# Kernel tuning notes

Measured on AMD Instinct MI355X. Metric: run time of the kernel, lower is better.

## Reference

```python
import jax, jax.numpy as jnp
import numpy as np
from jax import lax

NPOINT = 1024
RADIUS = 0.4
NSAMPLE = 32
BN_EPS = 1e-5


def _square_distance(src, dst):
    # src [B,S,3], dst [B,N,3] -> [B,S,N]
    d = -2.0 * jnp.einsum('bsc,bnc->bsn', src, dst)
    d = d + jnp.sum(src ** 2, -1)[:, :, None]
    d = d + jnp.sum(dst ** 2, -1)[:, None, :]
    return d


def _farthest_point_sample(xyz, npoint):
    # xyz [B,N,3] -> int32 indices [B,npoint]
    B, N, _ = xyz.shape
    # deterministic start at index 0 (torch uses randint; math is otherwise identical)
    init_far = jnp.zeros((B,), dtype=jnp.int32)
    init_dist = jnp.full((B, N), 1e10, dtype=xyz.dtype)

    def step(carry, _):
        distance, farthest = carry
        centroid = jnp.take_along_axis(xyz, farthest[:, None, None], axis=1)  # [B,1,3]
        dist = jnp.sum((xyz - centroid) ** 2, -1)  # [B,N]
        distance = jnp.minimum(distance, dist)
        new_far = jnp.argmax(distance, axis=-1).astype(jnp.int32)
        return (distance, new_far), farthest

    (_, _), cents = lax.scan(step, (init_dist, init_far), None, length=npoint)
    return cents.T  # [B, npoint]


def _query_ball_point(radius, nsample, xyz, new_xyz):
    # xyz [B,N,3], new_xyz [B,S,3] -> idx [B,S,nsample]
    B, N, _ = xyz.shape
    sqr = _square_distance(new_xyz, xyz)  # [B,S,N]
    ar = jnp.arange(N, dtype=jnp.int32)
    gi = jnp.where(sqr > radius * radius, N, ar[None, None, :])
    gi = jnp.sort(gi, axis=-1)[:, :, :nsample]
    first = gi[:, :, :1]
    return jnp.where(gi == N, first, gi)


def setup_inputs() -> dict:
    key = jax.random.key(0)
    ks = jax.random.split(key, 8)
    B, N = 16, 4096
    inp = {
        'xyz': jax.random.normal(ks[0], (B, 3, N), jnp.float32),
        'points': jax.random.normal(ks[1], (B, 6, N), jnp.float32),
    }
    dims = [(64, 9), (64, 64), (128, 64)]
    for i, (o, c) in enumerate(dims):
        inp[f'w{i}'] = jax.random.normal(ks[2 + i], (o, c), jnp.float32) * 0.05
        inp[f'b{i}'] = jnp.zeros((o,), jnp.float32)
        inp[f'g{i}'] = jnp.ones((o,), jnp.float32)
        inp[f'beta{i}'] = jnp.zeros((o,), jnp.float32)
    return inp


def reference(xyz, points, w0, b0, g0, beta0, w1, b1, g1, beta1, w2, b2, g2, beta2):
    # xyz [B,3,N], points [B,6,N]
    xyz_t = jnp.transpose(xyz, (0, 2, 1))      # [B,N,3]
    pts_t = jnp.transpose(points, (0, 2, 1))   # [B,N,6]
    B, N, _ = xyz_t.shape
    S, ns = NPOINT, NSAMPLE

    fps_idx = _farthest_point_sample(xyz_t, S)                 # [B,S]
    new_xyz = jnp.take_along_axis(xyz_t, fps_idx[:, :, None], axis=1)  # [B,S,3]
    idx = _query_ball_point(RADIUS, ns, xyz_t, new_xyz)        # [B,S,ns]
    flat = idx.reshape(B, S * ns, 1)
    g_xyz = jnp.take_along_axis(xyz_t, flat, axis=1).reshape(B, S, ns, 3)
    g_xyz = g_xyz - new_xyz[:, :, None, :]                     # grouped_xyz_norm
    g_pts = jnp.take_along_axis(pts_t, flat, axis=1).reshape(B, S, ns, -1)
    feat = jnp.concatenate([g_xyz, g_pts], axis=-1)            # [B,S,ns,9]

    # shared MLP: 1x1 conv + BatchNorm (training-mode batch stats) + ReLU
    for w, b, g, be in ((w0, b0, g0, beta0), (w1, b1, g1, beta1), (w2, b2, g2, beta2)):
        h = jnp.einsum('bsnc,oc->bsno', feat, w) + b
        mu = jnp.mean(h, axis=(0, 1, 2))
        var = jnp.var(h, axis=(0, 1, 2))
        feat = jax.nn.relu((h - mu) * lax.rsqrt(var + BN_EPS) * g + be)

    new_points = jnp.max(feat, axis=2)                         # max over nsample -> [B,S,Cout]
    return (jnp.transpose(new_xyz, (0, 2, 1)), jnp.transpose(new_points, (0, 2, 1)))
```

## Files before the change

kernel.cpp:

```cpp
#include <hip/hip_runtime.h>
#include <hip/hip_bf16.h>
#include <stdint.h>

#define NB 16
#define NP 4096
#define NSP 1024
#define KNN 32
#define PTOT (NB*NSP*KNN)
#define NTILES (PTOT/16)

typedef __attribute__((ext_vector_type(8))) short short8;
typedef __attribute__((ext_vector_type(4))) float f32x4;
typedef __attribute__((ext_vector_type(2))) float f32x2;

__device__ __forceinline__ float fadd_(float a,float b){return __fadd_rn(a,b);}
__device__ __forceinline__ float fmul_(float a,float b){return __fmul_rn(a,b);}
__device__ __forceinline__ float fsub_(float a,float b){return __fsub_rn(a,b);}

__device__ __forceinline__ float bf2f(unsigned short u){
    unsigned int x = ((unsigned int)u) << 16; float f; __builtin_memcpy(&f,&x,4); return f;
}
__device__ __forceinline__ unsigned short f2bf(float f){
    unsigned int x; __builtin_memcpy(&x,&f,4);
    x = x + 0x7fffu + ((x>>16)&1u);
    return (unsigned short)(x>>16);
}

template<int CTRL>
__device__ __forceinline__ float dpp_fmax_step(float v){
    int d = __builtin_amdgcn_update_dpp(0, __float_as_int(v), CTRL, 0xF, 0xF, true);
    return fmaxf(v, __int_as_float(d));
}

__device__ __forceinline__ void ab_from_stats(const double* __restrict__ st, const float* __restrict__ g,
    const float* __restrict__ beta, int o, float* A_out, float* B_out)
{
    double s=0.0, q=0.0;
#pragma unroll
    for (int slot=0;slot<8;slot++){
        s += st[(size_t)(slot*2+0)*128+o];
        q += st[(size_t)(slot*2+1)*128+o];
    }
    const double cnt = (double)PTOT;
    float mean = (float)(s/cnt);
    float var  = (float)(q/cnt - (s/cnt)*(s/cnt));
    float inv  = rsqrtf(var + 1e-5f);
    float A = g[o]*inv;
    *A_out = A; *B_out = beta[o] - mean*A;
}

__global__ __launch_bounds__(256,1) void fps_kernel(const float* __restrict__ xyz,
    float* __restrict__ new_xyz, float* __restrict__ out0)
{
    const int b = blockIdx.x, tid = threadIdx.x;
    const int lane = tid & 63, wv = tid >> 6;
    const float* xb = xyz + (size_t)b*3*NP;
    __shared__ float4 sp[NP];
    __shared__ unsigned long long slots[2][4];
    __shared__ int lds_far[NSP];
    f32x2 px[8], py[8], pz[8], pd2[8];
    const int base = tid*16;
#pragma unroll
    for (int j=0;j<16;j+=4){
        float4 vx = *(const float4*)(xb + base + j);
        float4 vy = *(const float4*)(xb + NP + base + j);
        float4 vz = *(const float4*)(xb + 2*NP + base + j);
        px[j/2]   = (f32x2){vx.x,vx.y}; px[j/2+1] = (f32x2){vx.z,vx.w};
        py[j/2]   = (f32x2){vy.x,vy.y}; py[j/2+1] = (f32x2){vy.z,vy.w};
        pz[j/2]   = (f32x2){vz.x,vz.y}; pz[j/2+1] = (f32x2){vz.z,vz.w};
        sp[base+j+0] = make_float4(vx.x,vy.x,vz.x,0.f);
        sp[base+j+1] = make_float4(vx.y,vy.y,vz.y,0.f);
        sp[base+j+2] = make_float4(vx.z,vy.z,vz.z,0.f);
        sp[base+j+3] = make_float4(vx.w,vy.w,vz.w,0.f);
        pd2[j/2]   = (f32x2){1e10f,1e10f};
        pd2[j/2+1] = (f32x2){1e10f,1e10f};
    }
    __syncthreads();
    int far = 0;
    float cx, cy, cz;
    { float4 c0 = sp[0]; cx=c0.x; cy=c0.y; cz=c0.z; }
    for (int s=0;s<NSP;s++){
        if (tid == (s & 255)) lds_far[s] = far;
        f32x2 bm2 = (f32x2){-1.f,-1.f};
        {
#pragma clang fp contract(off)
            const f32x2 cx2 = (f32x2){cx,cx}, cy2 = (f32x2){cy,cy}, cz2 = (f32x2){cz,cz};
#pragma unroll
            for (int k=0;k<8;k++){
                f32x2 dx = px[k]-cx2, dy = py[k]-cy2, dz = pz[k]-cz2;
                f32x2 d  = (dx*dx + dy*dy) + dz*dz;
                pd2[k] = __builtin_elementwise_min(pd2[k], d);
                bm2    = __builtin_elementwise_max(bm2, pd2[k]);
            }
        }
        float bd = fmaxf(bm2.x, bm2.y);
        float m = bd;
        m = dpp_fmax_step<0x111>(m);
        m = dpp_fmax_step<0x112>(m);
        m = dpp_fmax_step<0x114>(m);
        m = dpp_fmax_step<0x118>(m);
        m = dpp_fmax_step<0x142>(m);
        m = dpp_fmax_step<0x143>(m);
        const float wm = __int_as_float(__builtin_amdgcn_readlane(__float_as_int(m), 63));
        int il = 0;
#pragma unroll
        for (int k=7;k>=0;k--){
            if (pd2[k].y == wm) il = 2*k+1;
            if (pd2[k].x == wm) il = 2*k;
        }
        unsigned long long wmask = __ballot(bd == wm);
        int L = __ffsll(wmask) - 1;
        int widx = __builtin_amdgcn_readlane(base + il, L);
        unsigned long long key = ((unsigned long long)__float_as_uint(wm) << 32)
                               | (unsigned int)(NP-1-widx);
        if (lane==0) slots[s&1][wv] = key;
        __syncthreads();
        {
            const unsigned long long* sl = slots[s&1];
            unsigned long long a0 = sl[0], a1 = sl[1], a2 = sl[2], a3 = sl[3];
            unsigned long long m0 = a0>a1?a0:a1, m1 = a2>a3?a2:a3;
            unsigned long long mx = m0>m1?m0:m1;
            far = NP-1-(int)(mx & 0xFFFFFFFFu);
        }
        float4 c = sp[far]; cx=c.x; cy=c.y; cz=c.z;
    }
    __syncthreads();
    for (int i=tid;i<NSP;i+=256){
        int id = lds_far[i];
        float4 c = sp[id];
        float* nz = new_xyz + ((size_t)b*NSP + i)*3;
        nz[0]=c.x; nz[1]=c.y; nz[2]=c.z;
        out0[(size_t)b*3*NSP + i]         = c.x;
        out0[(size_t)b*3*NSP + NSP + i]   = c.y;
        out0[(size_t)b*3*NSP + 2*NSP + i] = c.z;
    }
}

__global__ __launch_bounds__(256,1) void ball_gather_kernel(const float* __restrict__ xyz,
    const float* __restrict__ pts, const float* __restrict__ new_xyz,
    unsigned short* __restrict__ feat)
{
    const int lane = threadIdx.x & 63, wv = threadIdx.x >> 6;
    const int center = blockIdx.x*4 + wv;
    const int b = center >> 10;
    const float* xb = xyz + (size_t)b*3*NP;
    const float* pb = pts + (size_t)b*6*NP;
    const float* nz = new_xyz + (size_t)center*3;
    const float cx=nz[0], cy=nz[1], cz=nz[2];
    const float src2 = fadd_(fadd_(fmul_(cx,cx),fmul_(cy,cy)),fmul_(cz,cz));
    const float R2 = (float)(0.4*0.4);
    __shared__ int slots[4][32];
    int total = 0;
    for (int c0=0;c0<NP;c0+=64){
        const int i = c0 + lane;
        float x=xb[i], y=xb[NP+i], z=xb[2*NP+i];
        float dot  = fadd_(fadd_(fmul_(cx,x),fmul_(cy,y)),fmul_(cz,z));
        float dst2 = fadd_(fadd_(fmul_(x,x),fmul_(y,y)),fmul_(z,z));
        float d = fadd_(fadd_(fmul_(-2.0f,dot), src2), dst2);
        bool pred = !(d > R2);
        unsigned long long m = __ballot(pred);
        int pos = total + (int)__popcll(m & ((1ull<<lane)-1ull));
        if (pred && pos < 32) slots[wv][pos] = i;
        total += (int)__popcll(m);
        if (total >= 32) break;
    }
    const int nvalid = total < 32 ? total : 32;
    const int n = lane & 31;
    const int idx = slots[wv][ (n < nvalid) ? n : 0 ];
    unsigned short* fr = feat + (size_t)center*KNN*32 + (size_t)n*32;
    if (lane < 32){
        float gx = fsub_(xb[idx], cx), gy = fsub_(xb[NP+idx], cy), gz = fsub_(xb[2*NP+idx], cz);
        float p0=pb[idx], p1=pb[NP+idx], p2=pb[2*NP+idx], p3=pb[3*NP+idx], p4=pb[4*NP+idx];
        short8 v;
        v[0]=(short)f2bf(gx); v[1]=(short)f2bf(gy); v[2]=(short)f2bf(gz);
        v[3]=(short)f2bf(p0); v[4]=(short)f2bf(p1); v[5]=(short)f2bf(p2);
        v[6]=(short)f2bf(p3); v[7]=(short)f2bf(p4);
        *(short8*)fr = v;
    } else {
        float p5 = pb[5*NP+idx];
        short8 v = (short8){0,0,0,0,0,0,0,0};
        v[0]=(short)f2bf(p5);
        *(short8*)(fr+8)  = v;
        short8 z8 = (short8){0,0,0,0,0,0,0,0};
        *(short8*)(fr+16) = z8;
        *(short8*)(fr+24) = z8;
    }
}

template<int KT,int OT,bool NORM_IN,bool STORE_H>
__global__ __launch_bounds__(256,1) void conv_kernel(const unsigned short* __restrict__ in,
    const unsigned short* __restrict__ wp, const float* __restrict__ bias,
    const double* __restrict__ stats_in, const float* __restrict__ gin,
    const float* __restrict__ bein,
    unsigned short* __restrict__ h_out, double* __restrict__ stats)
{
    constexpr int K = KT*32, O = OT*16;
    const int lane = threadIdx.x & 63, wv = threadIdx.x >> 6;
    const int col = lane & 15, quad = lane >> 4;
    __shared__ float sA[128], sB[128];
    if constexpr (NORM_IN){
        if ((int)threadIdx.x < K){
            float A, B;
            ab_from_stats(stats_in, gin, bein, threadIdx.x, &A, &B);
            sA[threadIdx.x] = A; sB[threadIdx.x] = B;
        }
        __syncthreads();
    }
    short8 bf[OT][KT];
#pragma unroll
    for (int t=0;t<OT;t++)
#pragma unroll
        for (int kt=0;kt<KT;kt++)
            bf[t][kt] = *(const short8*)(wp + (size_t)(t*16+col)*K + kt*32 + quad*8);
    float brow[OT];
#pragma unroll
    for (int t=0;t<OT;t++) brow[t] = bias[t*16+col];
    float nA[KT*8], nB[KT*8];
    if constexpr (NORM_IN){
#pragma unroll
        for (int kt=0;kt<KT;kt++)
#pragma unroll
            for (int j=0;j<8;j++){
                int c = kt*32+quad*8+j;
                nA[kt*8+j]=sA[c]; nB[kt*8+j]=sB[c];
            }
    }
    float ssum[OT], ssq[OT];
#pragma unroll
    for (int t=0;t<OT;t++){ ssum[t]=0.f; ssq[t]=0.f; }
    const int gw = blockIdx.x*4 + wv, nw = gridDim.x*4;
    for (int tile=gw; tile<NTILES; tile+=nw){
        const int row0 = tile*16;
        short8 af[KT];
#pragma unroll
        for (int kt=0;kt<KT;kt++){
            af[kt] = *(const short8*)(in + (size_t)(row0+col)*K + kt*32 + quad*8);
            if constexpr (NORM_IN){
#pragma unroll
                for (int j=0;j<8;j++){
                    float x = bf2f((unsigned short)af[kt][j]);
                    x = fmaxf(x*nA[kt*8+j]+nB[kt*8+j], 0.f);
                    af[kt][j] = (short)f2bf(x);
                }
            }
        }
        f32x4 acc[OT];
#pragma unroll
        for (int t=0;t<OT;t++) acc[t] = (f32x4){0.f,0.f,0.f,0.f};
#pragma unroll
        for (int kt=0;kt<KT;kt++)
#pragma unroll
            for (int t=0;t<OT;t++)
                acc[t] = __builtin_amdgcn_mfma_f32_16x16x32_bf16(af[kt], bf[t][kt], acc[t], 0,0,0);
#pragma unroll
        for (int t=0;t<OT;t++){
#pragma unroll
            for (int r=0;r<4;r++){
                float h = acc[t][r] + brow[t];
                if constexpr (STORE_H)
                    h_out[(size_t)(row0 + quad*4 + r)*O + t*16 + col] = f2bf(h);
                ssum[t] += h; ssq[t] = fmaf(h,h,ssq[t]);
            }
        }
    }
    __shared__ float bsum[128], bssq[128];
    for (int i=threadIdx.x;i<128;i+=256){ bsum[i]=0.f; bssq[i]=0.f; }
    __syncthreads();
#pragma unroll
    for (int t=0;t<OT;t++){
        float v = ssum[t]; v += __shfl_xor(v,16,64); v += __shfl_xor(v,32,64);
        float q = ssq[t];  q += __shfl_xor(q,16,64); q += __shfl_xor(q,32,64);
        if (quad==0){ atomicAdd(&bsum[t*16+col], v); atomicAdd(&bssq[t*16+col], q); }
    }
    __syncthreads();
    if ((int)threadIdx.x < O){
        const int slot = blockIdx.x & 7;
        atomicAdd(&stats[(size_t)(slot*2+0)*128 + threadIdx.x], (double)bsum[threadIdx.x]);
        atomicAdd(&stats[(size_t)(slot*2+1)*128 + threadIdx.x], (double)bssq[threadIdx.x]);
    }
}

__global__ __launch_bounds__(256,1) void conv01_kernel(
    const unsigned short* __restrict__ feat,
    const unsigned short* __restrict__ wp0, const float* __restrict__ b0v,
    const double* __restrict__ stats0, const float* __restrict__ g0v,
    const float* __restrict__ be0v,
    const unsigned short* __restrict__ wp1, const float* __restrict__ b1v,
    unsigned short* __restrict__ h1_out, double* __restrict__ stats1)
{
    const int lane = threadIdx.x & 63, wv = threadIdx.x >> 6;
    const int col = lane & 15, quad = lane >> 4;
    __shared__ float sA[64], sB[64];
    __shared__ unsigned short scratch[4][16*72];
    if ((int)threadIdx.x < 64){
        float A, B;
        ab_from_stats(stats0, g0v, be0v, threadIdx.x, &A, &B);
        sA[threadIdx.x] = A; sB[threadIdx.x] = B;
    }
    __syncthreads();
    short8 bf0[4];
#pragma unroll
    for (int t=0;t<4;t++)
        bf0[t] = *(const short8*)(wp0 + (size_t)(t*16+col)*32 + quad*8);
    short8 bf1[4][2];
#pragma unroll
    for (int t=0;t<4;t++)
#pragma unroll
        for (int kt=0;kt<2;kt++)
            bf1[t][kt] = *(const short8*)(wp1 + (size_t)(t*16+col)*64 + kt*32 + quad*8);
    float b0row[4], n0A[4], n0B[4], b1row[4];
#pragma unroll
    for (int t=0;t<4;t++){
        b0row[t] = b0v[t*16+col];
        n0A[t]   = sA[t*16+col];
        n0B[t]   = sB[t*16+col];
        b1row[t] = b1v[t*16+col];
    }
    float ssum[4], ssq[4];
#pragma unroll
    for (int t=0;t<4;t++){ ssum[t]=0.f; ssq[t]=0.f; }
    unsigned short* sw = scratch[wv];
    const int gw = blockIdx.x*4 + wv, nw = gridDim.x*4;
    for (int tile=gw; tile<NTILES; tile+=nw){
        const int row0 = tile*16;
        short8 af0 = *(const short8*)(feat + (size_t)(row0+col)*32 + quad*8);
        f32x4 acc0[4];
#pragma unroll
        for (int t=0;t<4;t++) acc0[t] = (f32x4){0.f,0.f,0.f,0.f};
#pragma unroll
        for (int t=0;t<4;t++)
            acc0[t] = __builtin_amdgcn_mfma_f32_16x16x32_bf16(af0, bf0[t], acc0[t], 0,0,0);
#pragma unroll
        for (int t=0;t<4;t++)
#pragma unroll
            for (int r=0;r<4;r++){
                float h = acc0[t][r] + b0row[t];
                unsigned short hb = f2bf(h);
                float x = fmaxf(bf2f(hb)*n0A[t] + n0B[t], 0.f);
                sw[(quad*4+r)*72 + t*16 + col] = f2bf(x);
            }
        short8 af1[2];
        af1[0] = *(const short8*)(&sw[(size_t)col*72 + quad*8]);
        af1[1] = *(const short8*)(&sw[(size_t)col*72 + 32 + quad*8]);
        f32x4 acc1[4];
#pragma unroll
        for (int t=0;t<4;t++) acc1[t] = (f32x4){0.f,0.f,0.f,0.f};
#pragma unroll
        for (int kt=0;kt<2;kt++)
#pragma unroll
            for (int t=0;t<4;t++)
                acc1[t] = __builtin_amdgcn_mfma_f32_16x16x32_bf16(af1[kt], bf1[t][kt], acc1[t], 0,0,0);
#pragma unroll
        for (int t=0;t<4;t++)
#pragma unroll
            for (int r=0;r<4;r++){
                float h = acc1[t][r] + b1row[t];
                h1_out[(size_t)(row0 + quad*4 + r)*64 + t*16 + col] = f2bf(h);
                ssum[t] += h; ssq[t] = fmaf(h,h,ssq[t]);
            }
    }
    __shared__ float bsum[64], bssq[64];
    for (int i=threadIdx.x;i<64;i+=256){ bsum[i]=0.f; bssq[i]=0.f; }
    __syncthreads();
#pragma unroll
    for (int t=0;t<4;t++){
        float v = ssum[t]; v += __shfl_xor(v,16,64); v += __shfl_xor(v,32,64);
        float q = ssq[t];  q += __shfl_xor(q,16,64); q += __shfl_xor(q,32,64);
        if (quad==0){ atomicAdd(&bsum[t*16+col], v); atomicAdd(&bssq[t*16+col], q); }
    }
    __syncthreads();
    if ((int)threadIdx.x < 64){
        const int slot = blockIdx.x & 7;
        atomicAdd(&stats1[(size_t)(slot*2+0)*128 + threadIdx.x], (double)bsum[threadIdx.x]);
        atomicAdd(&stats1[(size_t)(slot*2+1)*128 + threadIdx.x], (double)bssq[threadIdx.x]);
    }
}

__global__ __launch_bounds__(256,1) void conv_final_kernel(const unsigned short* __restrict__ in,
    const unsigned short* __restrict__ wp, const float* __restrict__ bias,
    const double* __restrict__ stats1, const float* __restrict__ g1v,
    const float* __restrict__ be1v,
    const double* __restrict__ stats2, const float* __restrict__ g2v,
    const float* __restrict__ be2v,
    float* __restrict__ out1)
{
    constexpr int KT=2, OT=8, K=64;
    const int lane = threadIdx.x & 63, wv = threadIdx.x >> 6;
    const int col = lane & 15, quad = lane >> 4;
    __shared__ float sInA[64], sInB[64], sOutA[128], sOutB[128];
    {
        const int t0 = threadIdx.x;
        if (t0 < 128){
            float A, B;
            ab_from_stats(stats2, g2v, be2v, t0, &A, &B);
            sOutA[t0] = A; sOutB[t0] = B;
        } else if (t0 < 192){
            float A, B;
            ab_from_stats(stats1, g1v, be1v, t0-128, &A, &B);
            sInA[t0-128] = A; sInB[t0-128] = B;
        }
        __syncthreads();
    }
    short8 bf[OT][KT];
#pragma unroll
    for (int t=0;t<OT;t++)
#pragma unroll
        for (int kt=0;kt<KT;kt++)
            bf[t][kt] = *(const short8*)(wp + (size_t)(t*16+col)*K + kt*32 + quad*8);
    float brow[OT], oA[OT], oB[OT];
#pragma unroll
    for (int t=0;t<OT;t++){
        brow[t] = bias[t*16+col];
        oA[t] = sOutA[t*16+col];
        oB[t] = sOutB[t*16+col];
    }
    float nA[16], nB[16];
#pragma unroll
    for (int kt=0;kt<2;kt++)
#pragma unroll
        for (int j=0;j<8;j++){
            int c = kt*32+quad*8+j;
            nA[kt*8+j]=sInA[c]; nB[kt*8+j]=sInB[c];
        }
    const int gw = blockIdx.x*4 + wv, nw = gridDim.x*4;
    for (int grp=gw; grp<NB*NSP; grp+=nw){
        float vmax[OT];
#pragma unroll
        for (int t=0;t<OT;t++) vmax[t]=0.f;
#pragma unroll
        for (int mt=0; mt<2; mt++){
            const int row0 = grp*32 + mt*16;
            short8 af[KT];
#pragma unroll
            for (int kt=0;kt<2;kt++){
                af[kt] = *(const short8*)(in + (size_t)(row0+col)*K + kt*32 + quad*8);
#pragma unroll
                for (int j=0;j<8;j++){
                    float x = bf2f((unsigned short)af[kt][j]);
                    x = fmaxf(x*nA[kt*8+j]+nB[kt*8+j], 0.f);
                    af[kt][j] = (short)f2bf(x);
                }
            }
            f32x4 acc[OT];
#pragma unroll
            for (int t=0;t<OT;t++) acc[t] = (f32x4){0.f,0.f,0.f,0.f};
#pragma unroll
            for (int kt=0;kt<2;kt++)
#pragma unroll
                for (int t=0;t<OT;t++)
                    acc[t] = __builtin_amdgcn_mfma_f32_16x16x32_bf16(af[kt], bf[t][kt], acc[t], 0,0,0);
#pragma unroll
            for (int t=0;t<OT;t++){
#pragma unroll
                for (int r=0;r<4;r++){
                    float h = acc[t][r] + brow[t];
                    float x = fmaxf(h*oA[t]+oB[t], 0.f);
                    vmax[t] = fmaxf(vmax[t], x);
                }
            }
        }
#pragma unroll
        for (int t=0;t<OT;t++){
            float v = vmax[t];
            v = fmaxf(v, __shfl_xor(v,16,64));
            v = fmaxf(v, __shfl_xor(v,32,64));
            if (quad==0){
                int o = t*16+col, bb = grp>>10, ss = grp&1023;
                out1[((size_t)bb*128+o)*NSP + ss] = v;
            }
        }
    }
}

__global__ void prep_kernel(const float* __restrict__ w0, const float* __restrict__ w1,
    const float* __restrict__ w2, unsigned short* __restrict__ wp0,
    unsigned short* __restrict__ wp1, unsigned short* __restrict__ wp2)
{
    int t = blockIdx.x*256 + threadIdx.x;
    if (t < 64*32){ int o=t>>5, c=t&31; wp0[t] = (c<9) ? f2bf(w0[o*9+c]) : (unsigned short)0; }
    if (t < 64*64)  wp1[t] = f2bf(w1[t]);
    if (t < 128*64) wp2[t] = f2bf(w2[t]);
}

extern "C" void kernel_launch(void* const* d_in, const int* in_sizes, int n_in,
                              void* d_out, int out_size, void* d_ws, size_t ws_size,
                              hipStream_t stream)
{
    (void)in_sizes; (void)n_in; (void)out_size; (void)ws_size;
    const float* xyz = (const float*)d_in[0];
    const float* pts = (const float*)d_in[1];
    const float* w0  = (const float*)d_in[2];
    const float* b0  = (const float*)d_in[3];
    const float* g0  = (const float*)d_in[4];
    const float* be0 = (const float*)d_in[5];
    const float* w1  = (const float*)d_in[6];
    const float* b1  = (const float*)d_in[7];
    const float* g1  = (const float*)d_in[8];
    const float* be1 = (const float*)d_in[9];
    const float* w2  = (const float*)d_in[10];
    const float* b2  = (const float*)d_in[11];
    const float* g2  = (const float*)d_in[12];
    const float* be2 = (const float*)d_in[13];

    char* ws = (char*)d_ws;
    size_t off = 0;
    auto alloc = [&](size_t sz)->char*{ char* p = ws + off; off = (off + sz + 255) & ~(size_t)255; return p; };
    float*          new_xyz = (float*)         alloc((size_t)NB*NSP*3*4);
    unsigned short* wp0     = (unsigned short*)alloc(64*32*2);
    unsigned short* wp1     = (unsigned short*)alloc(64*64*2);
    unsigned short* wp2     = (unsigned short*)alloc(128*64*2);
    double*         stats   = (double*)        alloc((size_t)3*8*2*128*8);
    unsigned short* feat    = (unsigned short*)alloc((size_t)PTOT*32*2);
    unsigned short* h1      = (unsigned short*)alloc((size_t)PTOT*64*2);

    float* out0 = (float*)d_out;
    float* out1 = out0 + (size_t)NB*3*NSP;

    hipMemsetAsync(stats, 0, (size_t)3*8*2*128*8, stream);
    prep_kernel<<<32,256,0,stream>>>(w0,w1,w2,wp0,wp1,wp2);
    fps_kernel<<<NB,256,0,stream>>>(xyz, new_xyz, out0);
    ball_gather_kernel<<<NB*NSP/4,256,0,stream>>>(xyz, pts, new_xyz, feat);
    conv_kernel<1,4,false,false><<<1024,256,0,stream>>>(feat, wp0, b0, nullptr, nullptr, nullptr, nullptr, stats);
    conv01_kernel<<<1024,256,0,stream>>>(feat, wp0, b0, stats, g0, be0, wp1, b1, h1, stats + 2048);
    conv_kernel<2,8,true,false><<<1024,256,0,stream>>>(h1, wp2, b2, stats + 2048, g1, be1, nullptr, stats + 4096);
    conv_final_kernel<<<2048,256,0,stream>>>(h1, wp2, b2, stats + 2048, g1, be1, stats + 4096, g2, be2, out1);
}
```

Before: 860.8 us.

## Fuse layer-3 conv stats pass with pooling via per-group max/min of pre-BN output

Layer 3 no longer runs a separate stats-only conv pass followed by a second conv pass. A single pass computes the layer-3 conv, accumulates the BN sums, and records the per-group max and min of the pre-normalisation outputs. A small finalize kernel then applies the affine BN and ReLU, choosing max or min by the sign of the scale, since the affine map is monotonic. This removes one full read of h1 and one set of MFMA work, but writes two extra 8 MB buffers and adds a kernel launch.

```diff
diff --git a/kernel.cpp b/kernel.cpp
--- a/kernel.cpp
+++ b/kernel.cpp
@@ -8,6 +8,7 @@
 #define KNN 32
 #define PTOT (NB*NSP*KNN)
 #define NTILES (PTOT/16)
+#define NGRP (NB*NSP)
 
 typedef __attribute__((ext_vector_type(8))) short short8;
 typedef __attribute__((ext_vector_type(4))) float f32x4;
@@ -376,44 +377,34 @@
     }
 }
 
-__global__ __launch_bounds__(256,1) void conv_final_kernel(const unsigned short* __restrict__ in,
-    const unsigned short* __restrict__ wp, const float* __restrict__ bias,
+__global__ __launch_bounds__(256,1) void conv2_stats_pool_kernel(
+    const unsigned short* __restrict__ in,
+    const unsigned short* __restrict__ wp,
+    const float* __restrict__ bias,
     const double* __restrict__ stats1, const float* __restrict__ g1v,
     const float* __restrict__ be1v,
-    const double* __restrict__ stats2, const float* __restrict__ g2v,
-    const float* __restrict__ be2v,
-    float* __restrict__ out1)
+    double* __restrict__ stats2,
+    float* __restrict__ hmax, float* __restrict__ hmin)
 {
     constexpr int KT=2, OT=8, K=64;
     const int lane = threadIdx.x & 63, wv = threadIdx.x >> 6;
     const int col = lane & 15, quad = lane >> 4;
-    __shared__ float sInA[64], sInB[64], sOutA[128], sOutB[128];
-    {
-        const int t0 = threadIdx.x;
-        if (t0 < 128){
-            float A, B;
-            ab_from_stats(stats2, g2v, be2v, t0, &A, &B);
-            sOutA[t0] = A; sOutB[t0] = B;
-        } else if (t0 < 192){
-            float A, B;
-            ab_from_stats(stats1, g1v, be1v, t0-128, &A, &B);
-            sInA[t0-128] = A; sInB[t0-128] = B;
-        }
-        __syncthreads();
-    }
+    __shared__ float sInA[64], sInB[64];
+    if ((int)threadIdx.x < 64){
+        float A, B;
+        ab_from_stats(stats1, g1v, be1v, threadIdx.x, &A, &B);
+        sInA[threadIdx.x] = A; sInB[threadIdx.x] = B;
+    }
+    __syncthreads();
     short8 bf[OT][KT];
 #pragma unroll
     for (int t=0;t<OT;t++)
 #pragma unroll
         for (int kt=0;kt<KT;kt++)
             bf[t][kt] = *(const short8*)(wp + (size_t)(t*16+col)*K + kt*32 + quad*8);
-    float brow[OT], oA[OT], oB[OT];
-#pragma unroll
-    for (int t=0;t<OT;t++){
-        brow[t] = bias[t*16+col];
-        oA[t] = sOutA[t*16+col];
-        oB[t] = sOutB[t*16+col];
-    }
+    float brow[OT];
+#pragma unroll
+    for (int t=0;t<OT;t++) brow[t] = bias[t*16+col];
     float nA[16], nB[16];
 #pragma unroll
     for (int kt=0;kt<2;kt++)
@@ -422,11 +413,14 @@
             int c = kt*32+quad*8+j;
             nA[kt*8+j]=sInA[c]; nB[kt*8+j]=sInB[c];
         }
+    float ssum[OT], ssq[OT];
+#pragma unroll
+    for (int t=0;t<OT;t++){ ssum[t]=0.f; ssq[t]=0.f; }
     const int gw = blockIdx.x*4 + wv, nw = gridDim.x*4;
-    for (int grp=gw; grp<NB*NSP; grp+=nw){
-        float vmax[OT];
-#pragma unroll
-        for (int t=0;t<OT;t++) vmax[t]=0.f;
+    for (int grp=gw; grp<NGRP; grp+=nw){
+        float hmx[OT], hmn[OT];
+#pragma unroll
+        for (int t=0;t<OT;t++){ hmx[t]=-3.402823466e38f; hmn[t]=3.402823466e38f; }
 #pragma unroll
         for (int mt=0; mt<2; mt++){
             const int row0 = grp*32 + mt*16;
@@ -454,21 +448,64 @@
 #pragma unroll
                 for (int r=0;r<4;r++){
                     float h = acc[t][r] + brow[t];
-                    float x = fmaxf(h*oA[t]+oB[t], 0.f);
-                    vmax[t] = fmaxf(vmax[t], x);
+                    ssum[t] += h; ssq[t] = fmaf(h,h,ssq[t]);
+                    hmx[t] = fmaxf(hmx[t], h);
+                    hmn[t] = fminf(hmn[t], h);
                 }
             }
         }
 #pragma unroll
         for (int t=0;t<OT;t++){
-            float v = vmax[t];
-            v = fmaxf(v, __shfl_xor(v,16,64));
-            v = fmaxf(v, __shfl_xor(v,32,64));
+            float x = hmx[t];
+            x = fmaxf(x, __shfl_xor(x,16,64));
+            x = fmaxf(x, __shfl_xor(x,32,64));
+            float n = hmn[t];
+            n = fminf(n, __shfl_xor(n,16,64));
+            n = fminf(n, __shfl_xor(n,32,64));
             if (quad==0){
-                int o = t*16+col, bb = grp>>10, ss = grp&1023;
-                out1[((size_t)bb*128+o)*NSP + ss] = v;
-            }
-        }
+                hmax[(size_t)grp*128 + t*16+col] = x;
+                hmin[(size_t)grp*128 + t*16+col] = n;
+            }
+        }
+    }
+    __shared__ float bsum[128], bssq[128];
+    for (int i=threadIdx.x;i<128;i+=256){ bsum[i]=0.f; bssq[i]=0.f; }
+    __syncthreads();
+#pragma unroll
+    for (int t=0;t<OT;t++){
+        float v = ssum[t]; v += __shfl_xor(v,16,64); v += __shfl_xor(v,32,64);
+        float q = ssq[t];  q += __shfl_xor(q,16,64); q += __shfl_xor(q,32,64);
+        if (quad==0){ atomicAdd(&bsum[t*16+col], v); atomicAdd(&bssq[t*16+col], q); }
+    }
+    __syncthreads();
+    if ((int)threadIdx.x < 128){
+        const int slot = blockIdx.x & 7;
+        atomicAdd(&stats2[(size_t)(slot*2+0)*128 + threadIdx.x], (double)bsum[threadIdx.x]);
+        atomicAdd(&stats2[(size_t)(slot*2+1)*128 + threadIdx.x], (double)bssq[threadIdx.x]);
+    }
+}
+
+__global__ __launch_bounds__(256,1) void pool_finalize_kernel(
+    const double* __restrict__ stats2, const float* __restrict__ g2v,
+    const float* __restrict__ be2v,
+    const float* __restrict__ hmax, const float* __restrict__ hmin,
+    float* __restrict__ out1)
+{
+    const int blk = blockIdx.x;
+    const int bb = blk >> 7, o = blk & 127;
+    __shared__ float sAB[2];
+    if (threadIdx.x == 0){
+        float A, B;
+        ab_from_stats(stats2, g2v, be2v, o, &A, &B);
+        sAB[0] = A; sAB[1] = B;
+    }
+    __syncthreads();
+    const float A = sAB[0], B = sAB[1];
+    for (int ss = threadIdx.x; ss < NSP; ss += 256){
+        const size_t g = (size_t)bb*NSP + ss;
+        float mx = hmax[g*128 + o], mn = hmin[g*128 + o];
+        float sel = (A >= 0.f) ? mx : mn;
+        out1[((size_t)bb*128 + o)*NSP + ss] = fmaxf(fmaf(sel, A, B), 0.f);
     }
 }
 
@@ -510,6 +547,8 @@
     unsigned short* wp1     = (unsigned short*)alloc(64*64*2);
     unsigned short* wp2     = (unsigned short*)alloc(128*64*2);
     double*         stats   = (double*)        alloc((size_t)3*8*2*128*8);
+    float*          hmax    = (float*)         alloc((size_t)NGRP*128*4);
+    float*          hmin    = (float*)         alloc((size_t)NGRP*128*4);
     unsigned short* feat    = (unsigned short*)alloc((size_t)PTOT*32*2);
     unsigned short* h1      = (unsigned short*)alloc((size_t)PTOT*64*2);
 
@@ -522,6 +561,6 @@
     ball_gather_kernel<<<NB*NSP/4,256,0,stream>>>(xyz, pts, new_xyz, feat);
     conv_kernel<1,4,false,false><<<1024,256,0,stream>>>(feat, wp0, b0, nullptr, nullptr, nullptr, nullptr, stats);
     conv01_kernel<<<1024,256,0,stream>>>(feat, wp0, b0, stats, g0, be0, wp1, b1, h1, stats + 2048);
-    conv_kernel<2,8,true,false><<<1024,256,0,stream>>>(h1, wp2, b2, stats + 2048, g1, be1, nullptr, stats + 4096);
-    conv_final_kernel<<<2048,256,0,stream>>>(h1, wp2, b2, stats + 2048, g1, be1, stats + 4096, g2, be2, out1);
-}
+    conv2_stats_pool_kernel<<<1024,256,0,stream>>>(h1, wp2, b2, stats + 2048, g1, be1, stats + 4096, hmax, hmin);
+    pool_finalize_kernel<<<NB*128,256,0,stream>>>(stats + 4096, g2, be2, hmax, hmin, out1);
+}
```

Result: no change. 871.6 us (+1.3%).

## Fuse layer-0 BatchNorm statistics into ball-gather kernel via MFMA

Applied to the files above, without the earlier changes.

The ball query and gather kernel now also runs the first 1x1 conv on the gathered features, using MFMA on an LDS copy of each center's 32x32 tile. It reduces per-channel sum and sum-of-squares through shuffles, LDS atomics and global double atomics. This removes the separate stats-only conv pass over feat, saving a full launch and a re-read of feat. In exchange the gather kernel does more work, uses more LDS, and issues more global atomics.

```diff
diff --git a/kernel.cpp b/kernel.cpp
--- a/kernel.cpp
+++ b/kernel.cpp
@@ -138,7 +138,8 @@
 
 __global__ __launch_bounds__(256,1) void ball_gather_kernel(const float* __restrict__ xyz,
     const float* __restrict__ pts, const float* __restrict__ new_xyz,
-    unsigned short* __restrict__ feat)
+    const unsigned short* __restrict__ wp0, const float* __restrict__ b0v,
+    unsigned short* __restrict__ feat, double* __restrict__ stats0)
 {
     const int lane = threadIdx.x & 63, wv = threadIdx.x >> 6;
     const int center = blockIdx.x*4 + wv;
@@ -149,7 +150,16 @@
     const float cx=nz[0], cy=nz[1], cz=nz[2];
     const float src2 = fadd_(fadd_(fmul_(cx,cx),fmul_(cy,cy)),fmul_(cz,cz));
     const float R2 = (float)(0.4*0.4);
+    const int col = lane & 15, quad = lane >> 4;
     __shared__ int slots[4][32];
+    __shared__ unsigned short ftile[4][32*40];
+    short8 bf0[4];
+#pragma unroll
+    for (int t=0;t<4;t++)
+        bf0[t] = *(const short8*)(wp0 + (size_t)(t*16+col)*32 + quad*8);
+    float brow[4];
+#pragma unroll
+    for (int t=0;t<4;t++) brow[t] = b0v[t*16+col];
     int total = 0;
     for (int c0=0;c0<NP;c0+=64){
         const int i = c0 + lane;
@@ -168,6 +178,7 @@
     const int n = lane & 31;
     const int idx = slots[wv][ (n < nvalid) ? n : 0 ];
     unsigned short* fr = feat + (size_t)center*KNN*32 + (size_t)n*32;
+    unsigned short* ft = ftile[wv];
     if (lane < 32){
         float gx = fsub_(xb[idx], cx), gy = fsub_(xb[NP+idx], cy), gz = fsub_(xb[2*NP+idx], cz);
         float p0=pb[idx], p1=pb[NP+idx], p2=pb[2*NP+idx], p3=pb[3*NP+idx], p4=pb[4*NP+idx];
@@ -176,14 +187,53 @@
         v[3]=(short)f2bf(p0); v[4]=(short)f2bf(p1); v[5]=(short)f2bf(p2);
         v[6]=(short)f2bf(p3); v[7]=(short)f2bf(p4);
         *(short8*)fr = v;
+        *(short8*)(&ft[n*40]) = v;
     } else {
         float p5 = pb[5*NP+idx];
         short8 v = (short8){0,0,0,0,0,0,0,0};
         v[0]=(short)f2bf(p5);
+        short8 z8 = (short8){0,0,0,0,0,0,0,0};
         *(short8*)(fr+8)  = v;
-        short8 z8 = (short8){0,0,0,0,0,0,0,0};
         *(short8*)(fr+16) = z8;
         *(short8*)(fr+24) = z8;
+        *(short8*)(&ft[n*40+8])  = v;
+        *(short8*)(&ft[n*40+16]) = z8;
+        *(short8*)(&ft[n*40+24]) = z8;
+    }
+    float ssum[4], ssq[4];
+#pragma unroll
+    for (int t=0;t<4;t++){ ssum[t]=0.f; ssq[t]=0.f; }
+#pragma unroll
+    for (int mt=0; mt<2; mt++){
+        short8 af = *(const short8*)(&ft[(size_t)(mt*16+col)*40 + quad*8]);
+        f32x4 acc[4];
+#pragma unroll
+        for (int t=0;t<4;t++) acc[t] = (f32x4){0.f,0.f,0.f,0.f};
+#pragma unroll
+        for (int t=0;t<4;t++)
+            acc[t] = __builtin_amdgcn_mfma_f32_16x16x32_bf16(af, bf0[t], acc[t], 0,0,0);
+#pragma unroll
+        for (int t=0;t<4;t++)
+#pragma unroll
+            for (int r=0;r<4;r++){
+                float h = acc[t][r] + brow[t];
+                ssum[t] += h; ssq[t] = fmaf(h,h,ssq[t]);
+            }
+    }
+    __shared__ float bsum[64], bssq[64];
+    for (int i=threadIdx.x;i<64;i+=256){ bsum[i]=0.f; bssq[i]=0.f; }
+    __syncthreads();
+#pragma unroll
+    for (int t=0;t<4;t++){
+        float v = ssum[t]; v += __shfl_xor(v,16,64); v += __shfl_xor(v,32,64);
+        float q = ssq[t];  q += __shfl_xor(q,16,64); q += __shfl_xor(q,32,64);
+        if (quad==0){ atomicAdd(&bsum[t*16+col], v); atomicAdd(&bssq[t*16+col], q); }
+    }
+    __syncthreads();
+    if ((int)threadIdx.x < 64){
+        const int slot = blockIdx.x & 7;
+        atomicAdd(&stats0[(size_t)(slot*2+0)*128 + threadIdx.x], (double)bsum[threadIdx.x]);
+        atomicAdd(&stats0[(size_t)(slot*2+1)*128 + threadIdx.x], (double)bssq[threadIdx.x]);
     }
 }
 
@@ -519,8 +569,7 @@
     hipMemsetAsync(stats, 0, (size_t)3*8*2*128*8, stream);
     prep_kernel<<<32,256,0,stream>>>(w0,w1,w2,wp0,wp1,wp2);
     fps_kernel<<<NB,256,0,stream>>>(xyz, new_xyz, out0);
-    ball_gather_kernel<<<NB*NSP/4,256,0,stream>>>(xyz, pts, new_xyz, feat);
-    conv_kernel<1,4,false,false><<<1024,256,0,stream>>>(feat, wp0, b0, nullptr, nullptr, nullptr, nullptr, stats);
+    ball_gather_kernel<<<NB*NSP/4,256,0,stream>>>(xyz, pts, new_xyz, wp0, b0, feat, stats);
     conv01_kernel<<<1024,256,0,stream>>>(feat, wp0, b0, stats, g0, be0, wp1, b1, h1, stats + 2048);
     conv_kernel<2,8,true,false><<<1024,256,0,stream>>>(h1, wp2, b2, stats + 2048, g1, be1, nullptr, stats + 4096);
     conv_final_kernel<<<2048,256,0,stream>>>(h1, wp2, b2, stats + 2048, g1, be1, stats + 4096, g2, be2, out1);
```

Measured after the change: 877.8 us. Within noise of the previous version (+2.0%).

## Fuse FPS and ball-query gather into one producer-consumer persistent kernel

Applied to the files above, without the earlier changes.

FPS and the ball-query gather now run in one launch. The first 16 blocks run farthest-point sampling and publish each centroid to global memory, plus a progress counter every 32 steps. The remaining blocks spin-wait on that counter and gather neighbourhoods for centroids as soon as they are ready. This overlaps the serial FPS with the gather work and removes a launch boundary. It relies on all 512 blocks being co-resident so the spinning consumers cannot starve the producers, and it adds atomic polling traffic.

```diff
diff --git a/kernel.cpp b/kernel.cpp
--- a/kernel.cpp
+++ b/kernel.cpp
@@ -8,6 +8,8 @@
 #define KNN 32
 #define PTOT (NB*NSP*KNN)
 #define NTILES (PTOT/16)
+#define GRID_FG 512
+#define GWORK (NB*NSP/4)
 
 typedef __attribute__((ext_vector_type(8))) short short8;
 typedef __attribute__((ext_vector_type(4))) float f32x4;
@@ -49,141 +51,164 @@
     *A_out = A; *B_out = beta[o] - mean*A;
 }
 
-__global__ __launch_bounds__(256,1) void fps_kernel(const float* __restrict__ xyz,
-    float* __restrict__ new_xyz, float* __restrict__ out0)
-{
-    const int b = blockIdx.x, tid = threadIdx.x;
+__global__ __launch_bounds__(256,1) void fps_gather_kernel(const float* __restrict__ xyz,
+    const float* __restrict__ pts, float* __restrict__ out0,
+    unsigned short* __restrict__ feat,
+    unsigned long long* __restrict__ pubXY, unsigned* __restrict__ pubZ,
+    unsigned* __restrict__ progress)
+{
+    __shared__ __align__(16) char smem[65536 + 64 + NSP*4];
+    const int tid = threadIdx.x;
     const int lane = tid & 63, wv = tid >> 6;
-    const float* xb = xyz + (size_t)b*3*NP;
-    __shared__ float4 sp[NP];
-    __shared__ unsigned long long slots[2][4];
-    __shared__ int lds_far[NSP];
-    f32x2 px[8], py[8], pz[8], pd2[8];
-    const int base = tid*16;
-#pragma unroll
-    for (int j=0;j<16;j+=4){
-        float4 vx = *(const float4*)(xb + base + j);
-        float4 vy = *(const float4*)(xb + NP + base + j);
-        float4 vz = *(const float4*)(xb + 2*NP + base + j);
-        px[j/2]   = (f32x2){vx.x,vx.y}; px[j/2+1] = (f32x2){vx.z,vx.w};
-        py[j/2]   = (f32x2){vy.x,vy.y}; py[j/2+1] = (f32x2){vy.z,vy.w};
-        pz[j/2]   = (f32x2){vz.x,vz.y}; pz[j/2+1] = (f32x2){vz.z,vz.w};
-        sp[base+j+0] = make_float4(vx.x,vy.x,vz.x,0.f);
-        sp[base+j+1] = make_float4(vx.y,vy.y,vz.y,0.f);
-        sp[base+j+2] = make_float4(vx.z,vy.z,vz.z,0.f);
-        sp[base+j+3] = make_float4(vx.w,vy.w,vz.w,0.f);
-        pd2[j/2]   = (f32x2){1e10f,1e10f};
-        pd2[j/2+1] = (f32x2){1e10f,1e10f};
-    }
-    __syncthreads();
-    int far = 0;
-    float cx, cy, cz;
-    { float4 c0 = sp[0]; cx=c0.x; cy=c0.y; cz=c0.z; }
-    for (int s=0;s<NSP;s++){
-        if (tid == (s & 255)) lds_far[s] = far;
-        f32x2 bm2 = (f32x2){-1.f,-1.f};
-        {
+
+    if (blockIdx.x < NB){
+        const int b = blockIdx.x;
+        const float* xb = xyz + (size_t)b*3*NP;
+        float4* sp = (float4*)smem;
+        unsigned long long* kslots = (unsigned long long*)(smem + 65536);
+        int* lds_far = (int*)(smem + 65536 + 64);
+        f32x2 px[8], py[8], pz[8], pd2[8];
+        const int base = tid*16;
+#pragma unroll
+        for (int j=0;j<16;j+=4){
+            float4 vx = *(const float4*)(xb + base + j);
+            float4 vy = *(const float4*)(xb + NP + base + j);
+            float4 vz = *(const float4*)(xb + 2*NP + base + j);
+            px[j/2]   = (f32x2){vx.x,vx.y}; px[j/2+1] = (f32x2){vx.z,vx.w};
+            py[j/2]   = (f32x2){vy.x,vy.y}; py[j/2+1] = (f32x2){vy.z,vy.w};
+            pz[j/2]   = (f32x2){vz.x,vz.y}; pz[j/2+1] = (f32x2){vz.z,vz.w};
+            sp[base+j+0] = make_float4(vx.x,vy.x,vz.x,0.f);
+            sp[base+j+1] = make_float4(vx.y,vy.y,vz.y,0.f);
+            sp[base+j+2] = make_float4(vx.z,vy.z,vz.z,0.f);
+            sp[base+j+3] = make_float4(vx.w,vy.w,vz.w,0.f);
+            pd2[j/2]   = (f32x2){1e10f,1e10f};
+            pd2[j/2+1] = (f32x2){1e10f,1e10f};
+        }
+        __syncthreads();
+        int far = 0;
+        float cx, cy, cz;
+        { float4 c0 = sp[0]; cx=c0.x; cy=c0.y; cz=c0.z; }
+        for (int s=0;s<NSP;s++){
+            if (tid == (s & 255)) lds_far[s] = far;
+            if (tid == 0){
+                unsigned long long xy = ((unsigned long long)__float_as_uint(cy)<<32)
+                                      | (unsigned long long)__float_as_uint(cx);
+                __hip_atomic_store(&pubXY[b*NSP+s], xy, __ATOMIC_RELAXED, __HIP_MEMORY_SCOPE_AGENT);
+                __hip_atomic_store(&pubZ[b*NSP+s], __float_as_uint(cz), __ATOMIC_RELAXED, __HIP_MEMORY_SCOPE_AGENT);
+                if ((s & 31) == 0 && s > 0)
+                    __hip_atomic_store(&progress[b*16], (unsigned)s, __ATOMIC_RELEASE, __HIP_MEMORY_SCOPE_AGENT);
+            }
+            f32x2 bm2 = (f32x2){-1.f,-1.f};
+            {
 #pragma clang fp contract(off)
-            const f32x2 cx2 = (f32x2){cx,cx}, cy2 = (f32x2){cy,cy}, cz2 = (f32x2){cz,cz};
-#pragma unroll
-            for (int k=0;k<8;k++){
-                f32x2 dx = px[k]-cx2, dy = py[k]-cy2, dz = pz[k]-cz2;
-                f32x2 d  = (dx*dx + dy*dy) + dz*dz;
-                pd2[k] = __builtin_elementwise_min(pd2[k], d);
-                bm2    = __builtin_elementwise_max(bm2, pd2[k]);
-            }
-        }
-        float bd = fmaxf(bm2.x, bm2.y);
-        float m = bd;
-        m = dpp_fmax_step<0x111>(m);
-        m = dpp_fmax_step<0x112>(m);
-        m = dpp_fmax_step<0x114>(m);
-        m = dpp_fmax_step<0x118>(m);
-        m = dpp_fmax_step<0x142>(m);
-        m = dpp_fmax_step<0x143>(m);
-        const float wm = __int_as_float(__builtin_amdgcn_readlane(__float_as_int(m), 63));
-        int il = 0;
-#pragma unroll
-        for (int k=7;k>=0;k--){
-            if (pd2[k].y == wm) il = 2*k+1;
-            if (pd2[k].x == wm) il = 2*k;
-        }
-        unsigned long long wmask = __ballot(bd == wm);
-        int L = __ffsll(wmask) - 1;
-        int widx = __builtin_amdgcn_readlane(base + il, L);
-        unsigned long long key = ((unsigned long long)__float_as_uint(wm) << 32)
-                               | (unsigned int)(NP-1-widx);
-        if (lane==0) slots[s&1][wv] = key;
+                const f32x2 cx2 = (f32x2){cx,cx}, cy2 = (f32x2){cy,cy}, cz2 = (f32x2){cz,cz};
+#pragma unroll
+                for (int k=0;k<8;k++){
+                    f32x2 dx = px[k]-cx2, dy = py[k]-cy2, dz = pz[k]-cz2;
+                    f32x2 d  = (dx*dx + dy*dy) + dz*dz;
+                    pd2[k] = __builtin_elementwise_min(pd2[k], d);
+                    bm2    = __builtin_elementwise_max(bm2, pd2[k]);
+                }
+            }
+            float bd = fmaxf(bm2.x, bm2.y);
+            float m = bd;
+            m = dpp_fmax_step<0x111>(m);
+            m = dpp_fmax_step<0x112>(m);
+            m = dpp_fmax_step<0x114>(m);
+            m = dpp_fmax_step<0x118>(m);
+            m = dpp_fmax_step<0x142>(m);
+            m = dpp_fmax_step<0x143>(m);
+            const float wm = __int_as_float(__builtin_amdgcn_readlane(__float_as_int(m), 63));
+            int il = 0;
+#pragma unroll
+            for (int k=7;k>=0;k--){
+                if (pd2[k].y == wm) il = 2*k+1;
+                if (pd2[k].x == wm) il = 2*k;
+            }
+            unsigned long long wmask = __ballot(bd == wm);
+            int L = __ffsll(wmask) - 1;
+            int widx = __builtin_amdgcn_readlane(base + il, L);
+            unsigned long long key = ((unsigned long long)__float_as_uint(wm) << 32)
+                                   | (unsigned int)(NP-1-widx);
+            if (lane==0) kslots[(s&1)*4 + wv] = key;
+            __syncthreads();
+            {
+                const unsigned long long* sl = kslots + (s&1)*4;
+                unsigned long long a0 = sl[0], a1 = sl[1], a2 = sl[2], a3 = sl[3];
+                unsigned long long m0 = a0>a1?a0:a1, m1 = a2>a3?a2:a3;
+                unsigned long long mx = m0>m1?m0:m1;
+                far = NP-1-(int)(mx & 0xFFFFFFFFu);
+            }
+            float4 c = sp[far]; cx=c.x; cy=c.y; cz=c.z;
+        }
+        if (tid==0)
+            __hip_atomic_store(&progress[b*16], (unsigned)NSP, __ATOMIC_RELEASE, __HIP_MEMORY_SCOPE_AGENT);
         __syncthreads();
-        {
-            const unsigned long long* sl = slots[s&1];
-            unsigned long long a0 = sl[0], a1 = sl[1], a2 = sl[2], a3 = sl[3];
-            unsigned long long m0 = a0>a1?a0:a1, m1 = a2>a3?a2:a3;
-            unsigned long long mx = m0>m1?m0:m1;
-            far = NP-1-(int)(mx & 0xFFFFFFFFu);
-        }
-        float4 c = sp[far]; cx=c.x; cy=c.y; cz=c.z;
-    }
-    __syncthreads();
-    for (int i=tid;i<NSP;i+=256){
-        int id = lds_far[i];
-        float4 c = sp[id];
-        float* nz = new_xyz + ((size_t)b*NSP + i)*3;
-        nz[0]=c.x; nz[1]=c.y; nz[2]=c.z;
-        out0[(size_t)b*3*NSP + i]         = c.x;
-        out0[(size_t)b*3*NSP + NSP + i]   = c.y;
-        out0[(size_t)b*3*NSP + 2*NSP + i] = c.z;
-    }
-}
-
-__global__ __launch_bounds__(256,1) void ball_gather_kernel(const float* __restrict__ xyz,
-    const float* __restrict__ pts, const float* __restrict__ new_xyz,
-    unsigned short* __restrict__ feat)
-{
-    const int lane = threadIdx.x & 63, wv = threadIdx.x >> 6;
-    const int center = blockIdx.x*4 + wv;
-    const int b = center >> 10;
-    const float* xb = xyz + (size_t)b*3*NP;
-    const float* pb = pts + (size_t)b*6*NP;
-    const float* nz = new_xyz + (size_t)center*3;
-    const float cx=nz[0], cy=nz[1], cz=nz[2];
-    const float src2 = fadd_(fadd_(fmul_(cx,cx),fmul_(cy,cy)),fmul_(cz,cz));
+        for (int i=tid;i<NSP;i+=256){
+            int id = lds_far[i];
+            float4 c = sp[id];
+            out0[(size_t)b*3*NSP + i]         = c.x;
+            out0[(size_t)b*3*NSP + NSP + i]   = c.y;
+            out0[(size_t)b*3*NSP + 2*NSP + i] = c.z;
+        }
+        return;
+    }
+
+    int* gslots = ((int*)smem) + wv*32;
+    const int gblk = blockIdx.x - NB;
     const float R2 = (float)(0.4*0.4);
-    __shared__ int slots[4][32];
-    int total = 0;
-    for (int c0=0;c0<NP;c0+=64){
-        const int i = c0 + lane;
-        float x=xb[i], y=xb[NP+i], z=xb[2*NP+i];
-        float dot  = fadd_(fadd_(fmul_(cx,x),fmul_(cy,y)),fmul_(cz,z));
-        float dst2 = fadd_(fadd_(fmul_(x,x),fmul_(y,y)),fmul_(z,z));
-        float d = fadd_(fadd_(fmul_(-2.0f,dot), src2), dst2);
-        bool pred = !(d > R2);
-        unsigned long long m = __ballot(pred);
-        int pos = total + (int)__popcll(m & ((1ull<<lane)-1ull));
-        if (pred && pos < 32) slots[wv][pos] = i;
-        total += (int)__popcll(m);
-        if (total >= 32) break;
-    }
-    const int nvalid = total < 32 ? total : 32;
-    const int n = lane & 31;
-    const int idx = slots[wv][ (n < nvalid) ? n : 0 ];
-    unsigned short* fr = feat + (size_t)center*KNN*32 + (size_t)n*32;
-    if (lane < 32){
-        float gx = fsub_(xb[idx], cx), gy = fsub_(xb[NP+idx], cy), gz = fsub_(xb[2*NP+idx], cz);
-        float p0=pb[idx], p1=pb[NP+idx], p2=pb[2*NP+idx], p3=pb[3*NP+idx], p4=pb[4*NP+idx];
-        short8 v;
-        v[0]=(short)f2bf(gx); v[1]=(short)f2bf(gy); v[2]=(short)f2bf(gz);
-        v[3]=(short)f2bf(p0); v[4]=(short)f2bf(p1); v[5]=(short)f2bf(p2);
-        v[6]=(short)f2bf(p3); v[7]=(short)f2bf(p4);
-        *(short8*)fr = v;
-    } else {
-        float p5 = pb[5*NP+idx];
-        short8 v = (short8){0,0,0,0,0,0,0,0};
-        v[0]=(short)f2bf(p5);
-        *(short8*)(fr+8)  = v;
-        short8 z8 = (short8){0,0,0,0,0,0,0,0};
-        *(short8*)(fr+16) = z8;
-        *(short8*)(fr+24) = z8;
+    for (int j = gblk; j < GWORK; j += (GRID_FG - NB)){
+        const int ord = j*4 + wv;
+        const int s = ord >> 4, b = ord & 15;
+        const int center = b*NSP + s;
+        for (;;){
+            unsigned p = __hip_atomic_load(&progress[b*16], __ATOMIC_ACQUIRE, __HIP_MEMORY_SCOPE_AGENT);
+            if (p > (unsigned)s) break;
+            __builtin_amdgcn_s_sleep(32);
+        }
+        unsigned long long xy = __hip_atomic_load(&pubXY[center], __ATOMIC_RELAXED, __HIP_MEMORY_SCOPE_AGENT);
+        unsigned zb           = __hip_atomic_load(&pubZ[center],  __ATOMIC_RELAXED, __HIP_MEMORY_SCOPE_AGENT);
+        const float cx = __uint_as_float((unsigned)xy);
+        const float cy = __uint_as_float((unsigned)(xy>>32));
+        const float cz = __uint_as_float(zb);
+        const float* xb = xyz + (size_t)b*3*NP;
+        const float* pb = pts + (size_t)b*6*NP;
+        const float src2 = fadd_(fadd_(fmul_(cx,cx),fmul_(cy,cy)),fmul_(cz,cz));
+        int total = 0;
+        for (int c0=0;c0<NP;c0+=64){
+            const int i = c0 + lane;
+            float x=xb[i], y=xb[NP+i], z=xb[2*NP+i];
+            float dot  = fadd_(fadd_(fmul_(cx,x),fmul_(cy,y)),fmul_(cz,z));
+            float dst2 = fadd_(fadd_(fmul_(x,x),fmul_(y,y)),fmul_(z,z));
+            float d = fadd_(fadd_(fmul_(-2.0f,dot), src2), dst2);
+            bool pred = !(d > R2);
+            unsigned long long m = __ballot(pred);
+            int pos = total + (int)__popcll(m & ((1ull<<lane)-1ull));
+            if (pred && pos < 32) gslots[pos] = i;
+            total += (int)__popcll(m);
+            if (total >= 32) break;
+        }
+        const int nvalid = total < 32 ? total : 32;
+        const int n = lane & 31;
+        const int idx = gslots[ (n < nvalid) ? n : 0 ];
+        unsigned short* fr = feat + (size_t)center*KNN*32 + (size_t)n*32;
+        if (lane < 32){
+            float gx = fsub_(xb[idx], cx), gy = fsub_(xb[NP+idx], cy), gz = fsub_(xb[2*NP+idx], cz);
+            float p0=pb[idx], p1=pb[NP+idx], p2=pb[2*NP+idx], p3=pb[3*NP+idx], p4=pb[4*NP+idx];
+            short8 v;
+            v[0]=(short)f2bf(gx); v[1]=(short)f2bf(gy); v[2]=(short)f2bf(gz);
+            v[3]=(short)f2bf(p0); v[4]=(short)f2bf(p1); v[5]=(short)f2bf(p2);
+            v[6]=(short)f2bf(p3); v[7]=(short)f2bf(p4);
+            *(short8*)fr = v;
+        } else {
+            float p5 = pb[5*NP+idx];
+            short8 v = (short8){0,0,0,0,0,0,0,0};
+            v[0]=(short)f2bf(p5);
+            *(short8*)(fr+8)  = v;
+            short8 z8 = (short8){0,0,0,0,0,0,0,0};
+            *(short8*)(fr+16) = z8;
+            *(short8*)(fr+24) = z8;
+        }
     }
 }
 
@@ -505,21 +530,22 @@
     char* ws = (char*)d_ws;
     size_t off = 0;
     auto alloc = [&](size_t sz)->char*{ char* p = ws + off; off = (off + sz + 255) & ~(size_t)255; return p; };
-    float*          new_xyz = (float*)         alloc((size_t)NB*NSP*3*4);
     unsigned short* wp0     = (unsigned short*)alloc(64*32*2);
     unsigned short* wp1     = (unsigned short*)alloc(64*64*2);
     unsigned short* wp2     = (unsigned short*)alloc(128*64*2);
     double*         stats   = (double*)        alloc((size_t)3*8*2*128*8);
+    unsigned*       progress= (unsigned*)      alloc((size_t)16*16*4);
+    unsigned long long* pubXY = (unsigned long long*)alloc((size_t)NB*NSP*8);
+    unsigned*       pubZ    = (unsigned*)      alloc((size_t)NB*NSP*4);
     unsigned short* feat    = (unsigned short*)alloc((size_t)PTOT*32*2);
     unsigned short* h1      = (unsigned short*)alloc((size_t)PTOT*64*2);
 
     float* out0 = (float*)d_out;
     float* out1 = out0 + (size_t)NB*3*NSP;
 
-    hipMemsetAsync(stats, 0, (size_t)3*8*2*128*8, stream);
+    hipMemsetAsync(stats, 0, (size_t)3*8*2*128*8 + 16*16*4, stream);
     prep_kernel<<<32,256,0,stream>>>(w0,w1,w2,wp0,wp1,wp2);
-    fps_kernel<<<NB,256,0,stream>>>(xyz, new_xyz, out0);
-    ball_gather_kernel<<<NB*NSP/4,256,0,stream>>>(xyz, pts, new_xyz, feat);
+    fps_gather_kernel<<<GRID_FG,256,0,stream>>>(xyz, pts, out0, feat, pubXY, pubZ, progress);
     conv_kernel<1,4,false,false><<<1024,256,0,stream>>>(feat, wp0, b0, nullptr, nullptr, nullptr, nullptr, stats);
     conv01_kernel<<<1024,256,0,stream>>>(feat, wp0, b0, stats, g0, be0, wp1, b1, h1, stats + 2048);
     conv_kernel<2,8,true,false><<<1024,256,0,stream>>>(h1, wp2, b2, stats + 2048, g1, be1, nullptr, stats + 4096);
```

Result: slower. 929.0 us (+7.9%).
